# Optimization experiments

Hardware: AMD Instinct MI355X
Metric: run time of the kernel (lower is better)

The kernel has to match this reference:

```python
import jax, jax.numpy as jnp
import numpy as np

# GNB per-element parameters [s, beta, R, C6] indexed by atomic number Z (rows not listed stay zero)
_ROWS = {
 1:[0.2772,1.7504,3.6516,95.99], 2:[0.2425,2.087,2.1843,40.67], 3:[0.3266,2.3073,1.2711,70.21],
 4:[0.3964,2.8811,3.3497,114.51], 5:[0.3121,2.6366,2.7079,152.36], 6:[0.2455,3.0189,1.8219,184.28],
 7:[0.2743,2.9432,2.4667,482.54], 8:[0.2577,2.7407,2.365,405.57], 9:[0.2791,2.5863,1.5062,218.45],
 10:[0.2378,2.5307,1.8233,174.81], 11:[0.2592,2.5679,1.3974,181.7], 12:[0.3837,2.9613,3.3515,263.02],
 13:[0.3013,3.2377,3.0102,228.1], 14:[0.3202,3.2749,3.1629,359.43], 15:[0.3399,3.7491,3.2554,3222.12],
 16:[0.3215,3.6718,2.9539,2144.49], 17:[0.3071,3.418,3.0368,2072.46], 18:[0.2752,3.3306,2.6598,1357.42],
 19:[0.2264,2.9736,4.0877,1406.65], 20:[0.4015,3.4464,4.1275,1058.36], 21:[0.9388,4.5955,9.7282,11498.73],
 22:[0.6048,3.5334,8.5322,3361.33], 23:[0.3678,3.068,7.2344,2095.91], 24:[0.2848,2.8393,5.3605,1049.31],
 25:[0.355,3.055,3.718,966.27], 26:[0.4406,3.2628,3.6408,1571.36], 27:[0.4124,3.2622,3.4961,1183.59],
 28:[0.3139,2.749,3.5108,787.76], 29:[0.3345,2.9097,3.0537,563.93], 30:[0.3391,2.9024,3.0261,592.91],
 31:[0.3146,3.3924,3.1735,430.82], 32:[0.3327,3.2804,3.1773,812.57], 33:[0.404,3.8757,3.8357,4533.53],
 34:[0.3343,3.8562,3.1109,3440.92], 35:[0.3242,3.7067,3.2122,3859.82], 36:[0.292,3.6457,2.8263,2729.6],
 37:[0.2677,3.4421,2.412,1864.19], 38:[0.3446,3.559,1.894,1175.73], 39:[1.0038,5.7293,11.2061,32141.18],
 40:[0.6146,5.075,6.821,27655.14], 41:[0.4244,3.7156,7.2367,2864.2], 42:[0.4882,3.6853,3.901,3563.45],
 43:[0.4439,3.6987,4.0857,3266.43], 44:[0.4736,3.7826,4.045,3967.23], 45:[0.4039,3.4706,3.4813,2233.82],
 46:[0.3188,3.3433,3.0487,1393.49], 47:[0.2948,3.1186,2.7795,1315.09], 48:[0.3012,3.0853,2.8673,1311.47],
 49:[0.3351,3.5452,3.3339,1460.56], 50:[0.3134,3.2997,3.0086,1662.99], 51:[0.4081,4.1277,3.9919,8089.97],
 52:[0.3585,4.1795,3.4209,6887.05], 53:[0.3574,4.0988,3.5649,8799.32], 54:[0.3134,4.0387,3.0288,6136.5],
 55:[0.2872,3.8468,2.262,3757.31], 56:[0.3788,4.0368,1.3837,2561.18], 57:[1.0851,6.1365,12.171,66580.83],
 72:[0.5577,5.213,6.0791,27593.76], 73:[0.5308,4.7637,5.7661,15364.65], 74:[0.3926,3.6018,3.6366,2734.5],
 75:[0.5351,3.9552,4.241,4801.82], 76:[0.4701,4.0278,4.1348,5685.94], 77:[0.3661,3.6123,3.4213,2786.0],
 78:[0.3411,3.6066,3.2486,2699.79], 79:[0.3164,3.3822,2.9588,2282.6], 80:[0.3047,3.375,2.9381,2476.79],
 81:[0.2802,3.3964,2.7711,2988.7], 82:[0.2682,3.2481,2.5816,2506.63], 83:[0.3876,4.1225,3.785,8916.84],
 84:[0.3679,4.2313,3.5381,8694.22], 85:[0.368,4.2455,3.6985,11821.61], 86:[0.3195,4.1784,3.0551,8410.64],
}
_TAB = np.zeros((87, 4), np.float32)
for _z, _v in _ROWS.items():
    _TAB[_z] = _v
GNB_TABLE = jnp.asarray(_TAB)
C_SP2 = jnp.asarray(np.array([0.2808, 3.0548, 2.2348, 429.69], np.float32))
C_SP3 = jnp.asarray(np.array([0.2455, 3.0189, 1.8219, 184.28], np.float32))
N_CN2 = jnp.asarray(np.array([0.2996, 3.02, 2.6454, 720.18], np.float32))
N_CN3 = jnp.asarray(np.array([0.2743, 2.9432, 2.4667, 482.54], np.float32))

BJ_A1, BJ_A2, BJ_ALPHA = 0.4, 4.0, 14.0
CUTOFF_LR, CUTOFF_START = 10.0, 8.0  # cutoff_start = cutoff_lr - 2.0


def _poly_envelope(x):
    # PolynomialCutoff.calculate_envelope with r_max=1, p=6:
    x6 = x ** 6
    env = 1.0 - 28.0 * x6 + 48.0 * x6 * x - 21.0 * x6 * x * x
    return env * (x < 1.0)


def _gnb_forward(lengths, Z, edge_index):
    n_nodes = Z.shape[0]
    sender, receiver = edge_index[0], edge_index[1]

    # coordination numbers via scatter-add on receiver
    cn = jnp.zeros((n_nodes,), jnp.int32).at[receiver].add(1)

    # species-indexed params with CN-adaptive selection for C and N
    params = GNB_TABLE[Z]  # [N, 4]
    c_params = jnp.where((cn <= 3)[:, None], C_SP2[None, :], C_SP3[None, :])
    n_params = jnp.where((cn <= 2)[:, None], N_CN2[None, :], N_CN3[None, :])
    params = jnp.where((Z == 6)[:, None], c_params, params)
    params = jnp.where((Z == 7)[:, None], n_params, params)

    R_i = params[:, 2]
    C6_i = params[:, 3]

    # geometric-mean combination rules per edge
    C6_ij = jnp.sqrt(C6_i[sender] * C6_i[receiver])
    R_ij = jnp.sqrt(R_i[sender] * R_i[receiver])

    r = lengths
    # BJ damping: f = 1 / (1 + 6 (r/r0)^(-alpha)), r0 = a1 sqrt(R_ij) + a2
    r0 = BJ_A1 * jnp.sqrt(R_ij) + BJ_A2
    f_damp = 1.0 / (1.0 + 6.0 * (r0 / r) ** BJ_ALPHA)

    e_edge = -C6_ij / (R_ij ** 6 + r ** 6) * f_damp

    # long-range polynomial cutoff switching from 1 at cutoff_start to 0 at cutoff_lr
    x = (r - CUTOFF_START) / (CUTOFF_LR - CUTOFF_START)
    env = jnp.where(r < CUTOFF_START, 1.0, _poly_envelope(x))
    e_edge = e_edge * env

    # scatter-sum to atoms; 0.5 to split symmetric pair energy over both directions
    node_energy = jnp.zeros((n_nodes,), e_edge.dtype).at[receiver].add(0.5 * e_edge)
    return node_energy


def setup_inputs() -> dict:
    key = jax.random.key(0)
    k1, k2, k3 = jax.random.split(key, 3)
    n_nodes, n_edges = 100000, 6400000
    Z = jax.random.randint(k1, (n_nodes,), 1, 87, dtype=jnp.int32)
    edge_index = jax.random.randint(k2, (2, n_edges), 0, n_nodes, dtype=jnp.int32)
    lengths = jax.random.uniform(k3, (n_edges,), jnp.float32, 1.0, 10.5)
    return {"Z": Z, "edge_index": edge_index, "lengths": lengths}


def reference(Z, edge_index, lengths):
    return _gnb_forward(lengths, Z, edge_index)
```

## Files before the change

### kernel.cpp

```cpp
#include <hip/hip_runtime.h>


#define B2SHIFT 10
#define B2SIZE  1024
#define TILE    4096
#define SBLK    512
#define ESLICES 32
#define MAXB    128

__device__ __constant__ float2 GNB_RC6[87] = {
    {0.f, 0.f},
    {3.6516f, 95.99f},   {2.1843f, 40.67f},   {1.2711f, 70.21f},
    {3.3497f, 114.51f},  {2.7079f, 152.36f},  {1.8219f, 184.28f},
    {2.4667f, 482.54f},  {2.365f, 405.57f},   {1.5062f, 218.45f},
    {1.8233f, 174.81f},  {1.3974f, 181.7f},   {3.3515f, 263.02f},
    {3.0102f, 228.1f},   {3.1629f, 359.43f},  {3.2554f, 3222.12f},
    {2.9539f, 2144.49f}, {3.0368f, 2072.46f}, {2.6598f, 1357.42f},
    {4.0877f, 1406.65f}, {4.1275f, 1058.36f}, {9.7282f, 11498.73f},
    {8.5322f, 3361.33f}, {7.2344f, 2095.91f}, {5.3605f, 1049.31f},
    {3.718f, 966.27f},   {3.6408f, 1571.36f}, {3.4961f, 1183.59f},
    {3.5108f, 787.76f},  {3.0537f, 563.93f},  {3.0261f, 592.91f},
    {3.1735f, 430.82f},  {3.1773f, 812.57f},  {3.8357f, 4533.53f},
    {3.1109f, 3440.92f}, {3.2122f, 3859.82f}, {2.8263f, 2729.6f},
    {2.412f, 1864.19f},  {1.894f, 1175.73f},  {11.2061f, 32141.18f},
    {6.821f, 27655.14f}, {7.2367f, 2864.2f},  {3.901f, 3563.45f},
    {4.0857f, 3266.43f}, {4.045f, 3967.23f},  {3.4813f, 2233.82f},
    {3.0487f, 1393.49f}, {2.7795f, 1315.09f}, {2.8673f, 1311.47f},
    {3.3339f, 1460.56f}, {3.0086f, 1662.99f}, {3.9919f, 8089.97f},
    {3.4209f, 6887.05f}, {3.5649f, 8799.32f}, {3.0288f, 6136.5f},
    {2.262f, 3757.31f},  {1.3837f, 2561.18f}, {12.171f, 66580.83f},
    {0.f,0.f},{0.f,0.f},{0.f,0.f},{0.f,0.f},{0.f,0.f},{0.f,0.f},{0.f,0.f},
    {0.f,0.f},{0.f,0.f},{0.f,0.f},{0.f,0.f},{0.f,0.f},{0.f,0.f},{0.f,0.f},
    {6.0791f, 27593.76f}, {5.7661f, 15364.65f}, {3.6366f, 2734.5f},
    {4.241f, 4801.82f},   {4.1348f, 5685.94f},  {3.4213f, 2786.0f},
    {3.2486f, 2699.79f},  {2.9588f, 2282.6f},   {2.9381f, 2476.79f},
    {2.7711f, 2988.7f},   {2.5816f, 2506.63f},  {3.785f, 8916.84f},
    {3.5381f, 8694.22f},  {3.6985f, 11821.61f}, {3.0551f, 8410.64f},
};

__global__ void gnb_init(const int* __restrict__ Z, unsigned* __restrict__ isCN,
                         int nw, int n_nodes, int* __restrict__ zp, int zwords) {
    int stride = gridDim.x * blockDim.x;
    int t0 = blockIdx.x * blockDim.x + threadIdx.x;
    for (int i = t0; i < zwords; i += stride) zp[i] = 0;
    for (int w = t0; w < nw; w += stride) {
        unsigned m = 0;
        int base = w << 5;
        int lim = n_nodes - base; if (lim > 32) lim = 32;
        for (int k = 0; k < lim; ++k) {
            int z = Z[base + k];
            if (z == 6 || z == 7) m |= (1u << k);
        }
        isCN[w] = m;
    }
}

__global__ void __launch_bounds__(SBLK)
gnb_scatter(const int* __restrict__ send, const int* __restrict__ recv,
            const float* __restrict__ len, const unsigned* __restrict__ isCN,
            int* __restrict__ cn,
            uint2* __restrict__ buckets, unsigned* __restrict__ cursor,
            uint4* __restrict__ ovrec, unsigned* __restrict__ ocur,
            int n_edges, int cap, unsigned ocap, int NB2) {
    __shared__ unsigned cnt[MAXB];
    __shared__ unsigned pos[MAXB];
    __shared__ unsigned startp[MAXB + 1];
    __shared__ unsigned gbase[MAXB];
    __shared__ uint2 srec[TILE];
    __shared__ unsigned char bmap[TILE];
    const int tid = threadIdx.x;
    const int e0  = blockIdx.x * TILE;

    for (int b = tid; b < MAXB; b += SBLK) { cnt[b] = 0; pos[b] = 0; }
    __syncthreads();

    #pragma unroll
    for (int k = 0; k < 2; ++k) {
        int base = e0 + (k * SBLK + tid) * 4;
        if (base + 3 < n_edges) {
            int4   rv = *(const int4*)(recv + base);
            float4 lv = *(const float4*)(len + base);
            int rr[4] = {rv.x, rv.y, rv.z, rv.w};
            float ll[4] = {lv.x, lv.y, lv.z, lv.w};
            #pragma unroll
            for (int j = 0; j < 4; ++j) {
                unsigned r = (unsigned)rr[j];
                if (ll[j] < 10.0f) atomicAdd(&cnt[r >> B2SHIFT], 1u);
                if ((isCN[r >> 5] >> (r & 31)) & 1u) atomicAdd(&cn[r], 1);
            }
        } else {
            int lim = n_edges - base; if (lim < 0) lim = 0; if (lim > 4) lim = 4;
            for (int j = 0; j < lim; ++j) {
                unsigned r = (unsigned)recv[base + j];
                if (len[base + j] < 10.0f) atomicAdd(&cnt[r >> B2SHIFT], 1u);
                if ((isCN[r >> 5] >> (r & 31)) & 1u) atomicAdd(&cn[r], 1);
            }
        }
    }
    __syncthreads();

    if (tid == 0) {
        unsigned acc = 0;
        for (int b = 0; b < NB2; ++b) { startp[b] = acc; acc += cnt[b]; }
        startp[NB2] = acc;
    }
    __syncthreads();
    if (tid < NB2) gbase[tid] = atomicAdd(&cursor[tid], cnt[tid]);
    __syncthreads();

    #pragma unroll
    for (int k = 0; k < 2; ++k) {
        int base = e0 + (k * SBLK + tid) * 4;
        if (base + 3 < n_edges) {
            int4   sv = *(const int4*)(send + base);
            int4   rv = *(const int4*)(recv + base);
            uint4  lv = *(const uint4*)(len + base);
            int ss[4] = {sv.x, sv.y, sv.z, sv.w};
            int rr[4] = {rv.x, rv.y, rv.z, rv.w};
            unsigned ll[4] = {lv.x, lv.y, lv.z, lv.w};
            #pragma unroll
            for (int j = 0; j < 4; ++j) {
                if (__uint_as_float(ll[j]) >= 10.0f) continue;
                unsigned r = (unsigned)rr[j];
                unsigned b = r >> B2SHIFT;
                unsigned slot = startp[b] + atomicAdd(&pos[b], 1u);
                srec[slot] = make_uint2((unsigned)ss[j] | ((r & (B2SIZE - 1)) << 17), ll[j]);
                bmap[slot] = (unsigned char)b;
            }
        } else {
            int lim = n_edges - base; if (lim < 0) lim = 0; if (lim > 4) lim = 4;
            for (int j = 0; j < lim; ++j) {
                unsigned lbits = ((const unsigned*)len)[base + j];
                if (__uint_as_float(lbits) >= 10.0f) continue;
                unsigned r = (unsigned)recv[base + j];
                unsigned b = r >> B2SHIFT;
                unsigned slot = startp[b] + atomicAdd(&pos[b], 1u);
                srec[slot] = make_uint2((unsigned)send[base + j] | ((r & (B2SIZE - 1)) << 17),
                                        lbits);
                bmap[slot] = (unsigned char)b;
            }
        }
    }
    __syncthreads();

    unsigned total = startp[NB2];
    for (unsigned i = tid; i < total; i += SBLK) {
        unsigned b = bmap[i];
        unsigned g = gbase[b] + (i - startp[b]);
        uint2 rec = srec[i];
        if (g < (unsigned)cap) {
            buckets[(size_t)b * cap + g] = rec;
        } else {
            unsigned o = atomicAdd(ocur, 1u);
            unsigned r = ((unsigned)b << B2SHIFT) | ((rec.x >> 17) & (B2SIZE - 1));
            if (o < ocap) ovrec[o] = make_uint4(r, rec.x & 0x1FFFFu, rec.y, 0u);
        }
    }
}

__global__ void gnb_params(const int* __restrict__ Z, const int* __restrict__ cn,
                           float2* __restrict__ P2, int n_nodes) {
    int i = blockIdx.x * blockDim.x + threadIdx.x;
    if (i >= n_nodes) return;
    int z = Z[i];
    float Rp, C6;
    if (z == 6) {
        if (cn[i] <= 3) { Rp = 2.2348f; C6 = 429.69f; }
        else            { Rp = 1.8219f; C6 = 184.28f; }
    } else if (z == 7) {
        if (cn[i] <= 2) { Rp = 2.6454f; C6 = 720.18f; }
        else            { Rp = 2.4667f; C6 = 482.54f; }
    } else {
        float2 rc = GNB_RC6[z];
        Rp = rc.x; C6 = rc.y;
    }
    P2[i] = make_float2(sqrtf(C6), sqrtf(sqrtf(Rp)));
}

__device__ __forceinline__ float gnb_energy_eval(float2 ps, float2 pr, float rlen) {
    float env;
    if (rlen < 8.0f) {
        env = 1.0f;
    } else {
        float x = (rlen - 8.0f) * 0.5f;
        float x2 = x * x;
        float x6 = x2 * x2 * x2;
        env = 1.0f - 28.0f * x6 + 48.0f * x6 * x - 21.0f * x6 * x2;
    }
    float sR  = ps.y * pr.y;
    float C6  = ps.x * pr.x;
    float Rij = sR * sR;
    float R3  = Rij * Rij * Rij;
    float R6  = R3 * R3;
    float r0  = 0.4f * sR + 4.0f;
    float t   = r0 / rlen;
    float t2 = t * t, t4 = t2 * t2, t8 = t4 * t4;
    float t14 = t8 * t4 * t2;
    float fd = 1.0f / (1.0f + 6.0f * t14);
    float rl2 = rlen * rlen;
    float r6 = rl2 * rl2 * rl2;
    return -0.5f * C6 / (R6 + r6) * fd * env;
}

__global__ void __launch_bounds__(256)
gnb_energy(const uint2* __restrict__ buckets, const unsigned* __restrict__ cursor,
           const float2* __restrict__ P2, float* __restrict__ rep,
           int cap, int n_nodes) {
    __shared__ float  acc[2][B2SIZE + 8];
    __shared__ float2 p2loc[B2SIZE];
    const int b   = blockIdx.x / ESLICES;
    const int sl  = blockIdx.x % ESLICES;
    const int tid = threadIdx.x;
    const int rr  = (tid >> 6) & 1;

    for (int i = tid; i < 2 * (B2SIZE + 8); i += 256) acc[0][i] = 0.0f;
    for (int i = tid; i < B2SIZE; i += 256) {
        int node = (b << B2SHIFT) + i;
        p2loc[i] = (node < n_nodes) ? P2[node] : make_float2(0.f, 0.f);
    }
    __syncthreads();

    unsigned count = cursor[b];
    if (count > (unsigned)cap) count = (unsigned)cap;
    unsigned seg = (count + ESLICES - 1) / ESLICES;
    unsigned st  = (unsigned)sl * seg;
    unsigned en  = st + seg; if (en > count) en = count;

    const uint2* src = buckets + (size_t)b * cap;
    for (unsigned i = st + tid; i < en; i += 256) {
        uint2 rec = src[i];
        unsigned s    = rec.x & 0x1FFFFu;
        unsigned rlow = (rec.x >> 17) & (B2SIZE - 1);
        float e = gnb_energy_eval(P2[s], p2loc[rlow], __uint_as_float(rec.y));
        atomicAdd(&acc[rr][rlow], e);
    }
    __syncthreads();

    float* dst = rep + (size_t)blockIdx.x * B2SIZE;
    for (int i = tid; i < B2SIZE; i += 256) dst[i] = acc[0][i] + acc[1][i];
}

__global__ void gnb_ovf_energy(const uint4* __restrict__ ovrec, const unsigned* __restrict__ ocur,
                               const float2* __restrict__ P2, float* __restrict__ ovf,
                               unsigned ocap) {
    unsigned n = *ocur; if (n > ocap) n = ocap;
    int stride = gridDim.x * blockDim.x;
    for (unsigned i = blockIdx.x * blockDim.x + threadIdx.x; i < n; i += stride) {
        uint4 rec = ovrec[i];
        float rlen = __uint_as_float(rec.z);
        if (rlen >= 10.0f) continue;
        float e = gnb_energy_eval(P2[rec.y], P2[rec.x], rlen);
        atomicAdd(&ovf[rec.x], e);
    }
}

__global__ void gnb_reduce(const float* __restrict__ rep, const float* __restrict__ ovf,
                           float* __restrict__ out, int n_nodes) {
    int i = blockIdx.x * blockDim.x + threadIdx.x;
    if (i >= n_nodes) return;
    int b = i >> B2SHIFT;
    int j = i & (B2SIZE - 1);
    const float* src = rep + ((size_t)b * ESLICES) * B2SIZE + j;
    float sum = ovf[i];
    #pragma unroll
    for (int s = 0; s < ESLICES; ++s) sum += src[(size_t)s * B2SIZE];
    out[i] = sum;
}

extern "C" void kernel_launch(void* const* d_in, const int* in_sizes, int n_in,
                              void* d_out, int out_size, void* d_ws, size_t ws_size,
                              hipStream_t stream) {
    const int*   Z    = (const int*)d_in[0];
    const int*   eidx = (const int*)d_in[1];
    const float* len  = (const float*)d_in[2];
    float*       out  = (float*)d_out;

    const int n_nodes = in_sizes[0];
    const int n_edges = in_sizes[2];
    const int* send = eidx;
    const int* recv = eidx + n_edges;

    const int NB2 = (n_nodes + B2SIZE - 1) >> B2SHIFT;
    const int nw  = (n_nodes + 31) >> 5;
    const int nwp = (nw + 7) & ~7;

    char* ws = (char*)d_ws;
    unsigned* cursor = (unsigned*)ws;
    unsigned* ocur   = (unsigned*)(ws + MAXB * 4);
    int*      cn     = (int*)(ws + (MAXB + 8) * 4);
    float*    ovf    = (float*)(ws + ((size_t)n_nodes + MAXB + 8) * 4);
    float2*   P2     = (float2*)(ws + ((size_t)2 * n_nodes + MAXB + 8) * 4);
    unsigned* isCN   = (unsigned*)(ws + ((size_t)4 * n_nodes + MAXB + 8) * 4);
    float*    rep    = (float*)((char*)isCN + (size_t)nwp * 4);
    size_t rep_w     = (size_t)NB2 * ESLICES * B2SIZE;
    char*     tail   = (char*)rep + rep_w * 4;

    size_t fixed_words = (size_t)4 * n_nodes + MAXB + 8 + nwp + rep_w;
    size_t total_words = ws_size / 4;
    size_t avail = total_words > fixed_words ? total_words - fixed_words : 0;
    size_t ovw = avail / 32;
    unsigned ocap = (unsigned)(ovw / 4);
    long cap = (long)((avail - ovw) / (2 * (size_t)NB2));
    if (cap > n_edges) cap = n_edges;
    if (cap < 0) cap = 0;
    uint4* ovrec   = (uint4*)tail;
    uint2* buckets = (uint2*)(tail + (size_t)ocap * 16);

    const int B = 256;
    int node_blocks = (n_nodes + B - 1) / B;
    int scat_blocks = (n_edges + TILE - 1) / TILE;
    int zero_words  = 2 * n_nodes + MAXB + 8;

    gnb_init<<<256, B, 0, stream>>>(Z, isCN, nw, n_nodes, (int*)ws, zero_words);
    gnb_scatter<<<scat_blocks, SBLK, 0, stream>>>(send, recv, len, isCN, cn, buckets,
                                                  cursor, ovrec, ocur, n_edges,
                                                  (int)cap, ocap, NB2);
    gnb_params<<<node_blocks, B, 0, stream>>>(Z, cn, P2, n_nodes);
    gnb_energy<<<NB2 * ESLICES, B, 0, stream>>>(buckets, cursor, P2, rep, (int)cap, n_nodes);
    gnb_ovf_energy<<<8, B, 0, stream>>>(ovrec, ocur, P2, ovf, ocap);
    gnb_reduce<<<node_blocks, B, 0, stream>>>(rep, ovf, out, n_nodes);
}
```

Measured before the change: 203.2 us.

## Compress per-node params to byte ids, fuse overflow energy, shrink scatter tiles

Per-node parameters are now stored as a one-byte type id (Z or a carbon/nitrogen coordination variant) looked up in a small shared table, instead of a float2 per node. This shrinks the random gathers done in the energy kernel. The separate overflow-energy kernel is merged into the energy launch as extra blocks. The scatter kernel keeps its loaded receivers and lengths in registers so they are not read twice, and it folds the prefix offsets into the count array. Tile, block and slice sizes are halved, and the energy loop reads two records per 16-byte load, which adds a table indirection and more blocks in the scatter stage.

```diff
diff --git a/kernel.cpp b/kernel.cpp
--- a/kernel.cpp
+++ b/kernel.cpp
@@ -3,10 +3,11 @@
 
 #define B2SHIFT 10
 #define B2SIZE  1024
-#define TILE    4096
-#define SBLK    512
-#define ESLICES 32
+#define TILE    2048
+#define SBLK    256
+#define ESLICES 16
 #define MAXB    128
+#define OVB     8
 
 __device__ __constant__ float2 GNB_RC6[87] = {
     {0.f, 0.f},
@@ -39,7 +40,8 @@
 };
 
 __global__ void gnb_init(const int* __restrict__ Z, unsigned* __restrict__ isCN,
-                         int nw, int n_nodes, int* __restrict__ zp, int zwords) {
+                         float2* __restrict__ PT, int nw, int n_nodes,
+                         int* __restrict__ zp, int zwords) {
     int stride = gridDim.x * blockDim.x;
     int t0 = blockIdx.x * blockDim.x + threadIdx.x;
     for (int i = t0; i < zwords; i += stride) zp[i] = 0;
@@ -53,128 +55,128 @@
         }
         isCN[w] = m;
     }
-}
-
-__global__ void __launch_bounds__(SBLK)
+    if (t0 < 91) {
+        float R, C6;
+        if      (t0 < 87)  { float2 rc = GNB_RC6[t0]; R = rc.x; C6 = rc.y; }
+        else if (t0 == 87) { R = 2.2348f; C6 = 429.69f; }
+        else if (t0 == 88) { R = 1.8219f; C6 = 184.28f; }
+        else if (t0 == 89) { R = 2.6454f; C6 = 720.18f; }
+        else               { R = 2.4667f; C6 = 482.54f; }
+        PT[t0] = make_float2(sqrtf(C6), sqrtf(sqrtf(R)));
+    }
+}
+
+__global__ void __launch_bounds__(SBLK, 8)
 gnb_scatter(const int* __restrict__ send, const int* __restrict__ recv,
             const float* __restrict__ len, const unsigned* __restrict__ isCN,
             int* __restrict__ cn,
             uint2* __restrict__ buckets, unsigned* __restrict__ cursor,
             uint4* __restrict__ ovrec, unsigned* __restrict__ ocur,
             int n_edges, int cap, unsigned ocap, int NB2) {
-    __shared__ unsigned cnt[MAXB];
-    __shared__ unsigned pos[MAXB];
-    __shared__ unsigned startp[MAXB + 1];
+    __shared__ unsigned cnt[MAXB + 1];
     __shared__ unsigned gbase[MAXB];
     __shared__ uint2 srec[TILE];
     __shared__ unsigned char bmap[TILE];
     const int tid = threadIdx.x;
     const int e0  = blockIdx.x * TILE;
 
-    for (int b = tid; b < MAXB; b += SBLK) { cnt[b] = 0; pos[b] = 0; }
-    __syncthreads();
+    for (int b = tid; b < MAXB + 1; b += SBLK) cnt[b] = 0;
+    __syncthreads();
+
+    unsigned rv[8];
+    float    lv[8];
 
     #pragma unroll
     for (int k = 0; k < 2; ++k) {
         int base = e0 + (k * SBLK + tid) * 4;
         if (base + 3 < n_edges) {
-            int4   rv = *(const int4*)(recv + base);
-            float4 lv = *(const float4*)(len + base);
-            int rr[4] = {rv.x, rv.y, rv.z, rv.w};
-            float ll[4] = {lv.x, lv.y, lv.z, lv.w};
-            #pragma unroll
+            int4   rr = *(const int4*)(recv + base);
+            float4 ll = *(const float4*)(len + base);
+            rv[k*4+0] = (unsigned)rr.x; lv[k*4+0] = ll.x;
+            rv[k*4+1] = (unsigned)rr.y; lv[k*4+1] = ll.y;
+            rv[k*4+2] = (unsigned)rr.z; lv[k*4+2] = ll.z;
+            rv[k*4+3] = (unsigned)rr.w; lv[k*4+3] = ll.w;
+        } else {
             for (int j = 0; j < 4; ++j) {
-                unsigned r = (unsigned)rr[j];
-                if (ll[j] < 10.0f) atomicAdd(&cnt[r >> B2SHIFT], 1u);
-                if ((isCN[r >> 5] >> (r & 31)) & 1u) atomicAdd(&cn[r], 1);
+                int e = base + j;
+                if (e < n_edges) { rv[k*4+j] = (unsigned)recv[e]; lv[k*4+j] = len[e]; }
+                else             { rv[k*4+j] = 0xFFFFFFFFu;       lv[k*4+j] = 1e30f; }
             }
-        } else {
-            int lim = n_edges - base; if (lim < 0) lim = 0; if (lim > 4) lim = 4;
-            for (int j = 0; j < lim; ++j) {
-                unsigned r = (unsigned)recv[base + j];
-                if (len[base + j] < 10.0f) atomicAdd(&cnt[r >> B2SHIFT], 1u);
-                if ((isCN[r >> 5] >> (r & 31)) & 1u) atomicAdd(&cn[r], 1);
-            }
-        }
-    }
+        }
+    }
+    #pragma unroll
+    for (int i = 0; i < 8; ++i) {
+        unsigned r = rv[i];
+        if (r == 0xFFFFFFFFu) continue;
+        if ((isCN[r >> 5] >> (r & 31)) & 1u) atomicAdd(&cn[r], 1);
+        if (lv[i] < 10.0f) atomicAdd(&cnt[r >> B2SHIFT], 1u);
+    }
+    __syncthreads();
+
+    if (tid < NB2) gbase[tid] = atomicAdd(&cursor[tid], cnt[tid]);
     __syncthreads();
 
     if (tid == 0) {
         unsigned acc = 0;
-        for (int b = 0; b < NB2; ++b) { startp[b] = acc; acc += cnt[b]; }
-        startp[NB2] = acc;
-    }
-    __syncthreads();
-    if (tid < NB2) gbase[tid] = atomicAdd(&cursor[tid], cnt[tid]);
+        for (int b = 0; b < NB2; ++b) {
+            unsigned c = cnt[b];
+            cnt[b] = acc;
+            gbase[b] -= acc;
+            acc += c;
+        }
+        cnt[NB2] = acc;
+    }
     __syncthreads();
 
     #pragma unroll
     for (int k = 0; k < 2; ++k) {
         int base = e0 + (k * SBLK + tid) * 4;
+        unsigned sv[4];
         if (base + 3 < n_edges) {
-            int4   sv = *(const int4*)(send + base);
-            int4   rv = *(const int4*)(recv + base);
-            uint4  lv = *(const uint4*)(len + base);
-            int ss[4] = {sv.x, sv.y, sv.z, sv.w};
-            int rr[4] = {rv.x, rv.y, rv.z, rv.w};
-            unsigned ll[4] = {lv.x, lv.y, lv.z, lv.w};
-            #pragma unroll
-            for (int j = 0; j < 4; ++j) {
-                if (__uint_as_float(ll[j]) >= 10.0f) continue;
-                unsigned r = (unsigned)rr[j];
-                unsigned b = r >> B2SHIFT;
-                unsigned slot = startp[b] + atomicAdd(&pos[b], 1u);
-                srec[slot] = make_uint2((unsigned)ss[j] | ((r & (B2SIZE - 1)) << 17), ll[j]);
-                bmap[slot] = (unsigned char)b;
-            }
+            int4 s4 = *(const int4*)(send + base);
+            sv[0]=(unsigned)s4.x; sv[1]=(unsigned)s4.y; sv[2]=(unsigned)s4.z; sv[3]=(unsigned)s4.w;
         } else {
-            int lim = n_edges - base; if (lim < 0) lim = 0; if (lim > 4) lim = 4;
-            for (int j = 0; j < lim; ++j) {
-                unsigned lbits = ((const unsigned*)len)[base + j];
-                if (__uint_as_float(lbits) >= 10.0f) continue;
-                unsigned r = (unsigned)recv[base + j];
-                unsigned b = r >> B2SHIFT;
-                unsigned slot = startp[b] + atomicAdd(&pos[b], 1u);
-                srec[slot] = make_uint2((unsigned)send[base + j] | ((r & (B2SIZE - 1)) << 17),
-                                        lbits);
-                bmap[slot] = (unsigned char)b;
-            }
-        }
-    }
-    __syncthreads();
-
-    unsigned total = startp[NB2];
+            for (int j = 0; j < 4; ++j)
+                sv[j] = (base + j < n_edges) ? (unsigned)send[base + j] : 0u;
+        }
+        #pragma unroll
+        for (int j = 0; j < 4; ++j) {
+            int i = k * 4 + j;
+            if (rv[i] == 0xFFFFFFFFu || lv[i] >= 10.0f) continue;
+            unsigned r = rv[i];
+            unsigned b = r >> B2SHIFT;
+            unsigned slot = atomicAdd(&cnt[b], 1u);
+            srec[slot] = make_uint2(sv[j] | ((r & (B2SIZE - 1)) << 17),
+                                    __float_as_uint(lv[i]));
+            bmap[slot] = (unsigned char)b;
+        }
+    }
+    __syncthreads();
+
+    unsigned total = cnt[NB2];
     for (unsigned i = tid; i < total; i += SBLK) {
         unsigned b = bmap[i];
-        unsigned g = gbase[b] + (i - startp[b]);
+        unsigned g = gbase[b] + i;
         uint2 rec = srec[i];
         if (g < (unsigned)cap) {
             buckets[(size_t)b * cap + g] = rec;
         } else {
             unsigned o = atomicAdd(ocur, 1u);
-            unsigned r = ((unsigned)b << B2SHIFT) | ((rec.x >> 17) & (B2SIZE - 1));
+            unsigned r = (b << B2SHIFT) | ((rec.x >> 17) & (B2SIZE - 1));
             if (o < ocap) ovrec[o] = make_uint4(r, rec.x & 0x1FFFFu, rec.y, 0u);
         }
     }
 }
 
 __global__ void gnb_params(const int* __restrict__ Z, const int* __restrict__ cn,
-                           float2* __restrict__ P2, int n_nodes) {
+                           unsigned char* __restrict__ pid, int n_nodes) {
     int i = blockIdx.x * blockDim.x + threadIdx.x;
     if (i >= n_nodes) return;
     int z = Z[i];
-    float Rp, C6;
-    if (z == 6) {
-        if (cn[i] <= 3) { Rp = 2.2348f; C6 = 429.69f; }
-        else            { Rp = 1.8219f; C6 = 184.28f; }
-    } else if (z == 7) {
-        if (cn[i] <= 2) { Rp = 2.6454f; C6 = 720.18f; }
-        else            { Rp = 2.4667f; C6 = 482.54f; }
-    } else {
-        float2 rc = GNB_RC6[z];
-        Rp = rc.x; C6 = rc.y;
-    }
-    P2[i] = make_float2(sqrtf(C6), sqrtf(sqrtf(Rp)));
+    int id = z;
+    if (z == 6)      id = (cn[i] <= 3) ? 87 : 88;
+    else if (z == 7) id = (cn[i] <= 2) ? 89 : 90;
+    pid[i] = (unsigned char)id;
 }
 
 __device__ __forceinline__ float gnb_energy_eval(float2 ps, float2 pr, float rlen) {
@@ -204,54 +206,73 @@
 
 __global__ void __launch_bounds__(256)
 gnb_energy(const uint2* __restrict__ buckets, const unsigned* __restrict__ cursor,
-           const float2* __restrict__ P2, float* __restrict__ rep,
-           int cap, int n_nodes) {
+           const float2* __restrict__ PT, const unsigned char* __restrict__ pid,
+           float* __restrict__ rep, float* __restrict__ ovf,
+           const uint4* __restrict__ ovrec, const unsigned* __restrict__ ocur,
+           unsigned ocap, int cap, int n_nodes, int nmain) {
     __shared__ float  acc[2][B2SIZE + 8];
     __shared__ float2 p2loc[B2SIZE];
-    const int b   = blockIdx.x / ESLICES;
-    const int sl  = blockIdx.x % ESLICES;
+    __shared__ float2 ptab[96];
     const int tid = threadIdx.x;
+    const int bid = blockIdx.x;
+    const int b   = bid / ESLICES;
     const int rr  = (tid >> 6) & 1;
 
-    for (int i = tid; i < 2 * (B2SIZE + 8); i += 256) acc[0][i] = 0.0f;
-    for (int i = tid; i < B2SIZE; i += 256) {
-        int node = (b << B2SHIFT) + i;
-        p2loc[i] = (node < n_nodes) ? P2[node] : make_float2(0.f, 0.f);
-    }
-    __syncthreads();
-
+    if (tid < 91) ptab[tid] = PT[tid];
+    if (bid < nmain) {
+        for (int i = tid; i < 2 * (B2SIZE + 8); i += 256) acc[0][i] = 0.0f;
+        for (int i = tid; i < B2SIZE; i += 256) {
+            int node = (b << B2SHIFT) + i;
+            p2loc[i] = (node < n_nodes) ? PT[pid[node]] : make_float2(0.f, 0.f);
+        }
+    }
+    __syncthreads();
+
+    if (bid >= nmain) {
+        unsigned n = *ocur; if (n > ocap) n = ocap;
+        unsigned t0 = (unsigned)(bid - nmain) * 256 + tid;
+        for (unsigned i = t0; i < n; i += OVB * 256) {
+            uint4 rec = ovrec[i];
+            float rlen = __uint_as_float(rec.z);
+            if (rlen >= 10.0f) continue;
+            float e = gnb_energy_eval(ptab[pid[rec.y]], ptab[pid[rec.x]], rlen);
+            atomicAdd(&ovf[rec.x], e);
+        }
+        return;
+    }
+
+    const int sl = bid % ESLICES;
     unsigned count = cursor[b];
     if (count > (unsigned)cap) count = (unsigned)cap;
-    unsigned seg = (count + ESLICES - 1) / ESLICES;
+    unsigned seg = (((count + ESLICES - 1) / ESLICES) + 1) & ~1u;
     unsigned st  = (unsigned)sl * seg;
     unsigned en  = st + seg; if (en > count) en = count;
 
     const uint2* src = buckets + (size_t)b * cap;
-    for (unsigned i = st + tid; i < en; i += 256) {
-        uint2 rec = src[i];
-        unsigned s    = rec.x & 0x1FFFFu;
-        unsigned rlow = (rec.x >> 17) & (B2SIZE - 1);
-        float e = gnb_energy_eval(P2[s], p2loc[rlow], __uint_as_float(rec.y));
-        atomicAdd(&acc[rr][rlow], e);
-    }
-    __syncthreads();
-
-    float* dst = rep + (size_t)blockIdx.x * B2SIZE;
+    for (unsigned i = st + 2 * tid; i < en; i += 512) {
+        if (i + 1 < en) {
+            uint4 q = *(const uint4*)(src + i);
+            {
+                unsigned s = q.x & 0x1FFFFu, rl = (q.x >> 17) & (B2SIZE - 1);
+                float e = gnb_energy_eval(ptab[pid[s]], p2loc[rl], __uint_as_float(q.y));
+                atomicAdd(&acc[rr][rl], e);
+            }
+            {
+                unsigned s = q.z & 0x1FFFFu, rl = (q.z >> 17) & (B2SIZE - 1);
+                float e = gnb_energy_eval(ptab[pid[s]], p2loc[rl], __uint_as_float(q.w));
+                atomicAdd(&acc[rr][rl], e);
+            }
+        } else {
+            uint2 rec = src[i];
+            unsigned s = rec.x & 0x1FFFFu, rl = (rec.x >> 17) & (B2SIZE - 1);
+            float e = gnb_energy_eval(ptab[pid[s]], p2loc[rl], __uint_as_float(rec.y));
+            atomicAdd(&acc[rr][rl], e);
+        }
+    }
+    __syncthreads();
+
+    float* dst = rep + (size_t)bid * B2SIZE;
     for (int i = tid; i < B2SIZE; i += 256) dst[i] = acc[0][i] + acc[1][i];
-}
-
-__global__ void gnb_ovf_energy(const uint4* __restrict__ ovrec, const unsigned* __restrict__ ocur,
-                               const float2* __restrict__ P2, float* __restrict__ ovf,
-                               unsigned ocap) {
-    unsigned n = *ocur; if (n > ocap) n = ocap;
-    int stride = gridDim.x * blockDim.x;
-    for (unsigned i = blockIdx.x * blockDim.x + threadIdx.x; i < n; i += stride) {
-        uint4 rec = ovrec[i];
-        float rlen = __uint_as_float(rec.z);
-        if (rlen >= 10.0f) continue;
-        float e = gnb_energy_eval(P2[rec.y], P2[rec.x], rlen);
-        atomicAdd(&ovf[rec.x], e);
-    }
 }
 
 __global__ void gnb_reduce(const float* __restrict__ rep, const float* __restrict__ ovf,
@@ -281,42 +302,54 @@
     const int* recv = eidx + n_edges;
 
     const int NB2 = (n_nodes + B2SIZE - 1) >> B2SHIFT;
-    const int nw  = (n_nodes + 31) >> 5;
-    const int nwp = (nw + 7) & ~7;
+    const size_t nw  = (size_t)(n_nodes + 31) >> 5;
+    const size_t nwp = (nw + 3) & ~3ull;
+    const size_t npidw = (((size_t)n_nodes + 3) / 4 + 3) & ~3ull;
+
+    size_t o_cursor = 0;
+    size_t o_ocur   = 128;
+    size_t o_cn     = 136;
+    size_t o_ovf    = o_cn + n_nodes;
+    size_t o_PT     = o_ovf + n_nodes;
+    size_t o_isCN   = o_PT + 192;
+    size_t o_pid    = o_isCN + nwp;
+    size_t o_rep    = (o_pid + npidw + 3) & ~3ull;
+    size_t rep_w    = (size_t)NB2 * ESLICES * B2SIZE;
+    size_t o_tail   = (o_rep + rep_w + 3) & ~3ull;
 
     char* ws = (char*)d_ws;
-    unsigned* cursor = (unsigned*)ws;
-    unsigned* ocur   = (unsigned*)(ws + MAXB * 4);
-    int*      cn     = (int*)(ws + (MAXB + 8) * 4);
-    float*    ovf    = (float*)(ws + ((size_t)n_nodes + MAXB + 8) * 4);
-    float2*   P2     = (float2*)(ws + ((size_t)2 * n_nodes + MAXB + 8) * 4);
-    unsigned* isCN   = (unsigned*)(ws + ((size_t)4 * n_nodes + MAXB + 8) * 4);
-    float*    rep    = (float*)((char*)isCN + (size_t)nwp * 4);
-    size_t rep_w     = (size_t)NB2 * ESLICES * B2SIZE;
-    char*     tail   = (char*)rep + rep_w * 4;
-
-    size_t fixed_words = (size_t)4 * n_nodes + MAXB + 8 + nwp + rep_w;
+    unsigned*      cursor = (unsigned*)(ws + o_cursor * 4);
+    unsigned*      ocur   = (unsigned*)(ws + o_ocur * 4);
+    int*           cn     = (int*)(ws + o_cn * 4);
+    float*         ovf    = (float*)(ws + o_ovf * 4);
+    float2*        PT     = (float2*)(ws + o_PT * 4);
+    unsigned*      isCN   = (unsigned*)(ws + o_isCN * 4);
+    unsigned char* pid    = (unsigned char*)(ws + o_pid * 4);
+    float*         rep    = (float*)(ws + o_rep * 4);
+
     size_t total_words = ws_size / 4;
-    size_t avail = total_words > fixed_words ? total_words - fixed_words : 0;
+    size_t avail = total_words > o_tail ? total_words - o_tail : 0;
     size_t ovw = avail / 32;
     unsigned ocap = (unsigned)(ovw / 4);
     long cap = (long)((avail - ovw) / (2 * (size_t)NB2));
-    if (cap > n_edges) cap = n_edges;
+    if (cap > n_edges) cap = (long)n_edges;
     if (cap < 0) cap = 0;
-    uint4* ovrec   = (uint4*)tail;
-    uint2* buckets = (uint2*)(tail + (size_t)ocap * 16);
+    cap &= ~1L;
+    uint4* ovrec   = (uint4*)(ws + o_tail * 4);
+    uint2* buckets = (uint2*)(ws + (o_tail + (size_t)ocap * 4) * 4);
 
     const int B = 256;
     int node_blocks = (n_nodes + B - 1) / B;
     int scat_blocks = (n_edges + TILE - 1) / TILE;
-    int zero_words  = 2 * n_nodes + MAXB + 8;
-
-    gnb_init<<<256, B, 0, stream>>>(Z, isCN, nw, n_nodes, (int*)ws, zero_words);
+    int zero_words  = (int)o_PT;
+    int nmain = NB2 * ESLICES;
+
+    gnb_init<<<1024, B, 0, stream>>>(Z, isCN, PT, (int)nw, n_nodes, (int*)ws, zero_words);
     gnb_scatter<<<scat_blocks, SBLK, 0, stream>>>(send, recv, len, isCN, cn, buckets,
                                                   cursor, ovrec, ocur, n_edges,
                                                   (int)cap, ocap, NB2);
-    gnb_params<<<node_blocks, B, 0, stream>>>(Z, cn, P2, n_nodes);
-    gnb_energy<<<NB2 * ESLICES, B, 0, stream>>>(buckets, cursor, P2, rep, (int)cap, n_nodes);
-    gnb_ovf_energy<<<8, B, 0, stream>>>(ovrec, ocur, P2, ovf, ocap);
+    gnb_params<<<node_blocks, B, 0, stream>>>(Z, cn, pid, n_nodes);
+    gnb_energy<<<nmain + OVB, B, 0, stream>>>(buckets, cursor, PT, pid, rep, ovf,
+                                              ovrec, ocur, ocap, (int)cap, n_nodes, nmain);
     gnb_reduce<<<node_blocks, B, 0, stream>>>(rep, ovf, out, n_nodes);
 }
```

New measurement: 224.6 us. +10.5%, slower.

## Fuse all stages into a cooperative persistent kernel with grid syncs

Applied to the files above, without the earlier changes.

Merges the init, scatter, params, energy, overflow and reduce kernels into one persistent cooperative kernel that separates phases with grid-wide syncs. Per-node parameters become a one-byte id into a 91-entry table held in shared memory, and energy slices per bucket drop from 32 to 16. The aim is to remove launch gaps and shrink parameter and reduction traffic. In exchange, the grid is capped at about 4 blocks per CU and the scatter phase loops over tiles, which may reduce parallelism, and grid syncs add overhead. If the cooperative launch fails, the kernel is launched once per phase instead.

```diff
diff --git a/kernel.cpp b/kernel.cpp
--- a/kernel.cpp
+++ b/kernel.cpp
@@ -1,12 +1,16 @@
 #include <hip/hip_runtime.h>
+#include <hip/hip_cooperative_groups.h>
+
+namespace cg = cooperative_groups;
 
 
 #define B2SHIFT 10
 #define B2SIZE  1024
 #define TILE    4096
 #define SBLK    512
-#define ESLICES 32
+#define ES      16
 #define MAXB    128
+#define OVB     8
 
 __device__ __constant__ float2 GNB_RC6[87] = {
     {0.f, 0.f},
@@ -38,145 +42,6 @@
     {3.5381f, 8694.22f},  {3.6985f, 11821.61f}, {3.0551f, 8410.64f},
 };
 
-__global__ void gnb_init(const int* __restrict__ Z, unsigned* __restrict__ isCN,
-                         int nw, int n_nodes, int* __restrict__ zp, int zwords) {
-    int stride = gridDim.x * blockDim.x;
-    int t0 = blockIdx.x * blockDim.x + threadIdx.x;
-    for (int i = t0; i < zwords; i += stride) zp[i] = 0;
-    for (int w = t0; w < nw; w += stride) {
-        unsigned m = 0;
-        int base = w << 5;
-        int lim = n_nodes - base; if (lim > 32) lim = 32;
-        for (int k = 0; k < lim; ++k) {
-            int z = Z[base + k];
-            if (z == 6 || z == 7) m |= (1u << k);
-        }
-        isCN[w] = m;
-    }
-}
-
-__global__ void __launch_bounds__(SBLK)
-gnb_scatter(const int* __restrict__ send, const int* __restrict__ recv,
-            const float* __restrict__ len, const unsigned* __restrict__ isCN,
-            int* __restrict__ cn,
-            uint2* __restrict__ buckets, unsigned* __restrict__ cursor,
-            uint4* __restrict__ ovrec, unsigned* __restrict__ ocur,
-            int n_edges, int cap, unsigned ocap, int NB2) {
-    __shared__ unsigned cnt[MAXB];
-    __shared__ unsigned pos[MAXB];
-    __shared__ unsigned startp[MAXB + 1];
-    __shared__ unsigned gbase[MAXB];
-    __shared__ uint2 srec[TILE];
-    __shared__ unsigned char bmap[TILE];
-    const int tid = threadIdx.x;
-    const int e0  = blockIdx.x * TILE;
-
-    for (int b = tid; b < MAXB; b += SBLK) { cnt[b] = 0; pos[b] = 0; }
-    __syncthreads();
-
-    #pragma unroll
-    for (int k = 0; k < 2; ++k) {
-        int base = e0 + (k * SBLK + tid) * 4;
-        if (base + 3 < n_edges) {
-            int4   rv = *(const int4*)(recv + base);
-            float4 lv = *(const float4*)(len + base);
-            int rr[4] = {rv.x, rv.y, rv.z, rv.w};
-            float ll[4] = {lv.x, lv.y, lv.z, lv.w};
-            #pragma unroll
-            for (int j = 0; j < 4; ++j) {
-                unsigned r = (unsigned)rr[j];
-                if (ll[j] < 10.0f) atomicAdd(&cnt[r >> B2SHIFT], 1u);
-                if ((isCN[r >> 5] >> (r & 31)) & 1u) atomicAdd(&cn[r], 1);
-            }
-        } else {
-            int lim = n_edges - base; if (lim < 0) lim = 0; if (lim > 4) lim = 4;
-            for (int j = 0; j < lim; ++j) {
-                unsigned r = (unsigned)recv[base + j];
-                if (len[base + j] < 10.0f) atomicAdd(&cnt[r >> B2SHIFT], 1u);
-                if ((isCN[r >> 5] >> (r & 31)) & 1u) atomicAdd(&cn[r], 1);
-            }
-        }
-    }
-    __syncthreads();
-
-    if (tid == 0) {
-        unsigned acc = 0;
-        for (int b = 0; b < NB2; ++b) { startp[b] = acc; acc += cnt[b]; }
-        startp[NB2] = acc;
-    }
-    __syncthreads();
-    if (tid < NB2) gbase[tid] = atomicAdd(&cursor[tid], cnt[tid]);
-    __syncthreads();
-
-    #pragma unroll
-    for (int k = 0; k < 2; ++k) {
-        int base = e0 + (k * SBLK + tid) * 4;
-        if (base + 3 < n_edges) {
-            int4   sv = *(const int4*)(send + base);
-            int4   rv = *(const int4*)(recv + base);
-            uint4  lv = *(const uint4*)(len + base);
-            int ss[4] = {sv.x, sv.y, sv.z, sv.w};
-            int rr[4] = {rv.x, rv.y, rv.z, rv.w};
-            unsigned ll[4] = {lv.x, lv.y, lv.z, lv.w};
-            #pragma unroll
-            for (int j = 0; j < 4; ++j) {
-                if (__uint_as_float(ll[j]) >= 10.0f) continue;
-                unsigned r = (unsigned)rr[j];
-                unsigned b = r >> B2SHIFT;
-                unsigned slot = startp[b] + atomicAdd(&pos[b], 1u);
-                srec[slot] = make_uint2((unsigned)ss[j] | ((r & (B2SIZE - 1)) << 17), ll[j]);
-                bmap[slot] = (unsigned char)b;
-            }
-        } else {
-            int lim = n_edges - base; if (lim < 0) lim = 0; if (lim > 4) lim = 4;
-            for (int j = 0; j < lim; ++j) {
-                unsigned lbits = ((const unsigned*)len)[base + j];
-                if (__uint_as_float(lbits) >= 10.0f) continue;
-                unsigned r = (unsigned)recv[base + j];
-                unsigned b = r >> B2SHIFT;
-                unsigned slot = startp[b] + atomicAdd(&pos[b], 1u);
-                srec[slot] = make_uint2((unsigned)send[base + j] | ((r & (B2SIZE - 1)) << 17),
-                                        lbits);
-                bmap[slot] = (unsigned char)b;
-            }
-        }
-    }
-    __syncthreads();
-
-    unsigned total = startp[NB2];
-    for (unsigned i = tid; i < total; i += SBLK) {
-        unsigned b = bmap[i];
-        unsigned g = gbase[b] + (i - startp[b]);
-        uint2 rec = srec[i];
-        if (g < (unsigned)cap) {
-            buckets[(size_t)b * cap + g] = rec;
-        } else {
-            unsigned o = atomicAdd(ocur, 1u);
-            unsigned r = ((unsigned)b << B2SHIFT) | ((rec.x >> 17) & (B2SIZE - 1));
-            if (o < ocap) ovrec[o] = make_uint4(r, rec.x & 0x1FFFFu, rec.y, 0u);
-        }
-    }
-}
-
-__global__ void gnb_params(const int* __restrict__ Z, const int* __restrict__ cn,
-                           float2* __restrict__ P2, int n_nodes) {
-    int i = blockIdx.x * blockDim.x + threadIdx.x;
-    if (i >= n_nodes) return;
-    int z = Z[i];
-    float Rp, C6;
-    if (z == 6) {
-        if (cn[i] <= 3) { Rp = 2.2348f; C6 = 429.69f; }
-        else            { Rp = 1.8219f; C6 = 184.28f; }
-    } else if (z == 7) {
-        if (cn[i] <= 2) { Rp = 2.6454f; C6 = 720.18f; }
-        else            { Rp = 2.4667f; C6 = 482.54f; }
-    } else {
-        float2 rc = GNB_RC6[z];
-        Rp = rc.x; C6 = rc.y;
-    }
-    P2[i] = make_float2(sqrtf(C6), sqrtf(sqrtf(Rp)));
-}
-
 __device__ __forceinline__ float gnb_energy_eval(float2 ps, float2 pr, float rlen) {
     float env;
     if (rlen < 8.0f) {
@@ -202,69 +67,220 @@
     return -0.5f * C6 / (R6 + r6) * fd * env;
 }
 
-__global__ void __launch_bounds__(256)
-gnb_energy(const uint2* __restrict__ buckets, const unsigned* __restrict__ cursor,
-           const float2* __restrict__ P2, float* __restrict__ rep,
-           int cap, int n_nodes) {
-    __shared__ float  acc[2][B2SIZE + 8];
-    __shared__ float2 p2loc[B2SIZE];
-    const int b   = blockIdx.x / ESLICES;
-    const int sl  = blockIdx.x % ESLICES;
-    const int tid = threadIdx.x;
-    const int rr  = (tid >> 6) & 1;
-
-    for (int i = tid; i < 2 * (B2SIZE + 8); i += 256) acc[0][i] = 0.0f;
-    for (int i = tid; i < B2SIZE; i += 256) {
-        int node = (b << B2SHIFT) + i;
-        p2loc[i] = (node < n_nodes) ? P2[node] : make_float2(0.f, 0.f);
+#define SMEM_BYTES 37952
+
+__global__ void __launch_bounds__(SBLK, 8)
+gnb_mega(const int* __restrict__ send, const int* __restrict__ recv,
+         const float* __restrict__ len, const int* __restrict__ Z,
+         float* __restrict__ out,
+         unsigned* __restrict__ cursor, unsigned* __restrict__ ocur,
+         int* __restrict__ cn, float* __restrict__ ovf,
+         float2* __restrict__ PT, unsigned* __restrict__ isCN,
+         unsigned char* __restrict__ pid, float* __restrict__ rep,
+         uint4* __restrict__ ovrec, uint2* __restrict__ buckets,
+         int n_nodes, int n_edges, int NB2, int nw,
+         int cap, unsigned ocap, int zwords, int ntiles,
+         int phase_lo, int phase_hi) {
+    __shared__ __align__(16) char smem[SMEM_BYTES];
+    unsigned*      s_cnt   = (unsigned*)smem;
+    unsigned*      s_gbase = (unsigned*)(smem + 528);
+    uint2*         s_srec  = (uint2*)(smem + 1056);
+    unsigned char* s_bmap  = (unsigned char*)(smem + 33824);
+    float*         e_acc   = (float*)smem;
+    float2*        e_p2    = (float2*)(smem + 8256);
+    float2*        e_ptab  = (float2*)(smem + 16448);
+
+    cg::grid_group grid = cg::this_grid();
+    const int tid  = threadIdx.x;
+    const int gtid = blockIdx.x * SBLK + tid;
+    const int gstr = gridDim.x * SBLK;
+
+    for (int phase = phase_lo; phase <= phase_hi; ++phase) {
+        if (phase == 0) {
+            int* zp = (int*)cursor;
+            for (int i = gtid; i < zwords; i += gstr) zp[i] = 0;
+            for (int w = gtid; w < nw; w += gstr) {
+                unsigned m = 0;
+                int base = w << 5;
+                int lim = n_nodes - base; if (lim > 32) lim = 32;
+                for (int k = 0; k < lim; ++k) {
+                    int z = Z[base + k];
+                    if (z == 6 || z == 7) m |= (1u << k);
+                }
+                isCN[w] = m;
+            }
+            if (gtid < 91) {
+                float R, C6;
+                if      (gtid < 87)  { float2 rc = GNB_RC6[gtid]; R = rc.x; C6 = rc.y; }
+                else if (gtid == 87) { R = 2.2348f; C6 = 429.69f; }
+                else if (gtid == 88) { R = 1.8219f; C6 = 184.28f; }
+                else if (gtid == 89) { R = 2.6454f; C6 = 720.18f; }
+                else                 { R = 2.4667f; C6 = 482.54f; }
+                PT[gtid] = make_float2(sqrtf(C6), sqrtf(sqrtf(R)));
+            }
+        } else if (phase == 1) {
+            for (int t = blockIdx.x; t < ntiles; t += gridDim.x) {
+                for (int b = tid; b < MAXB + 1; b += SBLK) s_cnt[b] = 0;
+                __syncthreads();
+                const int e0 = t * TILE;
+
+                #pragma unroll
+                for (int k = 0; k < 2; ++k) {
+                    int base = e0 + (k * SBLK + tid) * 4;
+                    if (base + 3 < n_edges) {
+                        int4   rr = *(const int4*)(recv + base);
+                        float4 ll = *(const float4*)(len + base);
+                        int rv[4] = {rr.x, rr.y, rr.z, rr.w};
+                        float lv[4] = {ll.x, ll.y, ll.z, ll.w};
+                        #pragma unroll
+                        for (int j = 0; j < 4; ++j) {
+                            unsigned r = (unsigned)rv[j];
+                            if ((isCN[r >> 5] >> (r & 31)) & 1u) atomicAdd(&cn[r], 1);
+                            if (lv[j] < 10.0f) atomicAdd(&s_cnt[r >> B2SHIFT], 1u);
+                        }
+                    } else {
+                        int lim = n_edges - base; if (lim < 0) lim = 0; if (lim > 4) lim = 4;
+                        for (int j = 0; j < lim; ++j) {
+                            unsigned r = (unsigned)recv[base + j];
+                            if ((isCN[r >> 5] >> (r & 31)) & 1u) atomicAdd(&cn[r], 1);
+                            if (len[base + j] < 10.0f) atomicAdd(&s_cnt[r >> B2SHIFT], 1u);
+                        }
+                    }
+                }
+                __syncthreads();
+
+                if (tid < NB2) s_gbase[tid] = atomicAdd(&cursor[tid], s_cnt[tid]);
+                __syncthreads();
+                if (tid == 0) {
+                    unsigned acc = 0;
+                    for (int b = 0; b < NB2; ++b) {
+                        unsigned c = s_cnt[b];
+                        s_cnt[b] = acc;
+                        s_gbase[b] -= acc;
+                        acc += c;
+                    }
+                    s_cnt[NB2] = acc;
+                }
+                __syncthreads();
+
+                #pragma unroll
+                for (int k = 0; k < 2; ++k) {
+                    int base = e0 + (k * SBLK + tid) * 4;
+                    if (base + 3 < n_edges) {
+                        int4   sv = *(const int4*)(send + base);
+                        int4   rr = *(const int4*)(recv + base);
+                        uint4  ll = *(const uint4*)(len + base);
+                        int ss[4] = {sv.x, sv.y, sv.z, sv.w};
+                        int rv[4] = {rr.x, rr.y, rr.z, rr.w};
+                        unsigned lv[4] = {ll.x, ll.y, ll.z, ll.w};
+                        #pragma unroll
+                        for (int j = 0; j < 4; ++j) {
+                            if (__uint_as_float(lv[j]) >= 10.0f) continue;
+                            unsigned r = (unsigned)rv[j];
+                            unsigned b = r >> B2SHIFT;
+                            unsigned slot = atomicAdd(&s_cnt[b], 1u);
+                            s_srec[slot] = make_uint2((unsigned)ss[j] | ((r & (B2SIZE - 1)) << 17),
+                                                      lv[j]);
+                            s_bmap[slot] = (unsigned char)b;
+                        }
+                    } else {
+                        int lim = n_edges - base; if (lim < 0) lim = 0; if (lim > 4) lim = 4;
+                        for (int j = 0; j < lim; ++j) {
+                            unsigned lbits = ((const unsigned*)len)[base + j];
+                            if (__uint_as_float(lbits) >= 10.0f) continue;
+                            unsigned r = (unsigned)recv[base + j];
+                            unsigned b = r >> B2SHIFT;
+                            unsigned slot = atomicAdd(&s_cnt[b], 1u);
+                            s_srec[slot] = make_uint2((unsigned)send[base + j] |
+                                                      ((r & (B2SIZE - 1)) << 17), lbits);
+                            s_bmap[slot] = (unsigned char)b;
+                        }
+                    }
+                }
+                __syncthreads();
+
+                unsigned total = s_cnt[NB2];
+                for (unsigned i = tid; i < total; i += SBLK) {
+                    unsigned b = s_bmap[i];
+                    unsigned g = s_gbase[b] + i;
+                    uint2 rec = s_srec[i];
+                    if (g < (unsigned)cap) {
+                        buckets[(size_t)b * cap + g] = rec;
+                    } else {
+                        unsigned o = atomicAdd(ocur, 1u);
+                        unsigned r = ((unsigned)b << B2SHIFT) | ((rec.x >> 17) & (B2SIZE - 1));
+                        if (o < ocap) ovrec[o] = make_uint4(r, rec.x & 0x1FFFFu, rec.y, 0u);
+                    }
+                }
+            }
+        } else if (phase == 2) {
+            for (int i = gtid; i < n_nodes; i += gstr) {
+                int z = Z[i];
+                int id = z;
+                if (z == 6)      id = (cn[i] <= 3) ? 87 : 88;
+                else if (z == 7) id = (cn[i] <= 2) ? 89 : 90;
+                pid[i] = (unsigned char)id;
+            }
+        } else if (phase == 3) {
+            const int nmain = NB2 * ES;
+            for (int item = blockIdx.x; item < nmain + OVB; item += gridDim.x) {
+                if (item >= nmain) {
+                    unsigned n = *ocur; if (n > ocap) n = ocap;
+                    for (unsigned i = (unsigned)(item - nmain) * SBLK + tid; i < n;
+                         i += OVB * SBLK) {
+                        uint4 rec = ovrec[i];
+                        float rlen = __uint_as_float(rec.z);
+                        if (rlen >= 10.0f) continue;
+                        float e = gnb_energy_eval(PT[pid[rec.y]], PT[pid[rec.x]], rlen);
+                        atomicAdd(&ovf[rec.x], e);
+                    }
+                    continue;
+                }
+                const int b  = item / ES;
+                const int sl = item % ES;
+                if (tid < 91) e_ptab[tid] = PT[tid];
+                for (int i = tid; i < 2 * (B2SIZE + 8); i += SBLK) e_acc[i] = 0.0f;
+                for (int i = tid; i < B2SIZE; i += SBLK) {
+                    int node = (b << B2SHIFT) + i;
+                    e_p2[i] = (node < n_nodes) ? PT[pid[node]] : make_float2(0.f, 0.f);
+                }
+                __syncthreads();
+
+                unsigned count = cursor[b];
+                if (count > (unsigned)cap) count = (unsigned)cap;
+                unsigned seg = (count + ES - 1) / ES;
+                unsigned st  = (unsigned)sl * seg;
+                unsigned en  = st + seg; if (en > count) en = count;
+                const uint2* src = buckets + (size_t)b * cap;
+                const int rr = (tid >> 6) & 1;
+                for (unsigned i = st + tid; i < en; i += SBLK) {
+                    uint2 rec = src[i];
+                    unsigned s  = rec.x & 0x1FFFFu;
+                    unsigned rl = (rec.x >> 17) & (B2SIZE - 1);
+                    float e = gnb_energy_eval(e_ptab[pid[s]], e_p2[rl],
+                                              __uint_as_float(rec.y));
+                    atomicAdd(&e_acc[rr * (B2SIZE + 8) + rl], e);
+                }
+                __syncthreads();
+
+                float* dst = rep + (size_t)item * B2SIZE;
+                for (int i = tid; i < B2SIZE; i += SBLK)
+                    dst[i] = e_acc[i] + e_acc[B2SIZE + 8 + i];
+                __syncthreads();
+            }
+        } else {
+            for (int i = gtid; i < n_nodes; i += gstr) {
+                int b = i >> B2SHIFT;
+                int j = i & (B2SIZE - 1);
+                const float* src = rep + ((size_t)b * ES) * B2SIZE + j;
+                float sum = ovf[i];
+                #pragma unroll
+                for (int s = 0; s < ES; ++s) sum += src[(size_t)s * B2SIZE];
+                out[i] = sum;
+            }
+        }
+        if (phase < phase_hi) grid.sync();
     }
-    __syncthreads();
-
-    unsigned count = cursor[b];
-    if (count > (unsigned)cap) count = (unsigned)cap;
-    unsigned seg = (count + ESLICES - 1) / ESLICES;
-    unsigned st  = (unsigned)sl * seg;
-    unsigned en  = st + seg; if (en > count) en = count;
-
-    const uint2* src = buckets + (size_t)b * cap;
-    for (unsigned i = st + tid; i < en; i += 256) {
-        uint2 rec = src[i];
-        unsigned s    = rec.x & 0x1FFFFu;
-        unsigned rlow = (rec.x >> 17) & (B2SIZE - 1);
-        float e = gnb_energy_eval(P2[s], p2loc[rlow], __uint_as_float(rec.y));
-        atomicAdd(&acc[rr][rlow], e);
-    }
-    __syncthreads();
-
-    float* dst = rep + (size_t)blockIdx.x * B2SIZE;
-    for (int i = tid; i < B2SIZE; i += 256) dst[i] = acc[0][i] + acc[1][i];
-}
-
-__global__ void gnb_ovf_energy(const uint4* __restrict__ ovrec, const unsigned* __restrict__ ocur,
-                               const float2* __restrict__ P2, float* __restrict__ ovf,
-                               unsigned ocap) {
-    unsigned n = *ocur; if (n > ocap) n = ocap;
-    int stride = gridDim.x * blockDim.x;
-    for (unsigned i = blockIdx.x * blockDim.x + threadIdx.x; i < n; i += stride) {
-        uint4 rec = ovrec[i];
-        float rlen = __uint_as_float(rec.z);
-        if (rlen >= 10.0f) continue;
-        float e = gnb_energy_eval(P2[rec.y], P2[rec.x], rlen);
-        atomicAdd(&ovf[rec.x], e);
-    }
-}
-
-__global__ void gnb_reduce(const float* __restrict__ rep, const float* __restrict__ ovf,
-                           float* __restrict__ out, int n_nodes) {
-    int i = blockIdx.x * blockDim.x + threadIdx.x;
-    if (i >= n_nodes) return;
-    int b = i >> B2SHIFT;
-    int j = i & (B2SIZE - 1);
-    const float* src = rep + ((size_t)b * ESLICES) * B2SIZE + j;
-    float sum = ovf[i];
-    #pragma unroll
-    for (int s = 0; s < ESLICES; ++s) sum += src[(size_t)s * B2SIZE];
-    out[i] = sum;
 }
 
 extern "C" void kernel_launch(void* const* d_in, const int* in_sizes, int n_in,
@@ -272,51 +288,82 @@
                               hipStream_t stream) {
     const int*   Z    = (const int*)d_in[0];
     const int*   eidx = (const int*)d_in[1];
-    const float* len  = (const float*)d_in[2];
+    const float* lenp = (const float*)d_in[2];
     float*       out  = (float*)d_out;
 
-    const int n_nodes = in_sizes[0];
-    const int n_edges = in_sizes[2];
+    int n_nodes = in_sizes[0];
+    int n_edges = in_sizes[2];
     const int* send = eidx;
     const int* recv = eidx + n_edges;
 
-    const int NB2 = (n_nodes + B2SIZE - 1) >> B2SHIFT;
-    const int nw  = (n_nodes + 31) >> 5;
-    const int nwp = (nw + 7) & ~7;
+    int NB2 = (n_nodes + B2SIZE - 1) >> B2SHIFT;
+    int nw  = (n_nodes + 31) >> 5;
+    size_t nwp   = ((size_t)nw + 3) & ~3ull;
+    size_t npidw = (((size_t)n_nodes + 3) / 4 + 3) & ~3ull;
+
+    size_t o_cn   = 136;
+    size_t o_ovf  = o_cn + n_nodes;
+    size_t o_PT   = o_ovf + n_nodes;
+    size_t o_isCN = o_PT + 192;
+    size_t o_pid  = o_isCN + nwp;
+    size_t o_rep  = (o_pid + npidw + 3) & ~3ull;
+    size_t rep_w  = (size_t)NB2 * ES * B2SIZE;
+    size_t o_tail = (o_rep + rep_w + 3) & ~3ull;
 
     char* ws = (char*)d_ws;
-    unsigned* cursor = (unsigned*)ws;
-    unsigned* ocur   = (unsigned*)(ws + MAXB * 4);
-    int*      cn     = (int*)(ws + (MAXB + 8) * 4);
-    float*    ovf    = (float*)(ws + ((size_t)n_nodes + MAXB + 8) * 4);
-    float2*   P2     = (float2*)(ws + ((size_t)2 * n_nodes + MAXB + 8) * 4);
-    unsigned* isCN   = (unsigned*)(ws + ((size_t)4 * n_nodes + MAXB + 8) * 4);
-    float*    rep    = (float*)((char*)isCN + (size_t)nwp * 4);
-    size_t rep_w     = (size_t)NB2 * ESLICES * B2SIZE;
-    char*     tail   = (char*)rep + rep_w * 4;
-
-    size_t fixed_words = (size_t)4 * n_nodes + MAXB + 8 + nwp + rep_w;
+    unsigned*      cursor = (unsigned*)ws;
+    unsigned*      ocur   = (unsigned*)(ws + 128 * 4);
+    int*           cn     = (int*)(ws + o_cn * 4);
+    float*         ovf    = (float*)(ws + o_ovf * 4);
+    float2*        PT     = (float2*)(ws + o_PT * 4);
+    unsigned*      isCN   = (unsigned*)(ws + o_isCN * 4);
+    unsigned char* pid    = (unsigned char*)(ws + o_pid * 4);
+    float*         rep    = (float*)(ws + o_rep * 4);
+
     size_t total_words = ws_size / 4;
-    size_t avail = total_words > fixed_words ? total_words - fixed_words : 0;
+    size_t avail = total_words > o_tail ? total_words - o_tail : 0;
     size_t ovw = avail / 32;
     unsigned ocap = (unsigned)(ovw / 4);
     long cap = (long)((avail - ovw) / (2 * (size_t)NB2));
     if (cap > n_edges) cap = n_edges;
     if (cap < 0) cap = 0;
-    uint4* ovrec   = (uint4*)tail;
-    uint2* buckets = (uint2*)(tail + (size_t)ocap * 16);
-
-    const int B = 256;
-    int node_blocks = (n_nodes + B - 1) / B;
-    int scat_blocks = (n_edges + TILE - 1) / TILE;
-    int zero_words  = 2 * n_nodes + MAXB + 8;
-
-    gnb_init<<<256, B, 0, stream>>>(Z, isCN, nw, n_nodes, (int*)ws, zero_words);
-    gnb_scatter<<<scat_blocks, SBLK, 0, stream>>>(send, recv, len, isCN, cn, buckets,
-                                                  cursor, ovrec, ocur, n_edges,
-                                                  (int)cap, ocap, NB2);
-    gnb_params<<<node_blocks, B, 0, stream>>>(Z, cn, P2, n_nodes);
-    gnb_energy<<<NB2 * ESLICES, B, 0, stream>>>(buckets, cursor, P2, rep, (int)cap, n_nodes);
-    gnb_ovf_energy<<<8, B, 0, stream>>>(ovrec, ocur, P2, ovf, ocap);
-    gnb_reduce<<<node_blocks, B, 0, stream>>>(rep, ovf, out, n_nodes);
+    uint4* ovrec   = (uint4*)(ws + o_tail * 4);
+    uint2* buckets = (uint2*)(ws + (o_tail + (size_t)ocap * 4) * 4);
+
+    int zwords = (int)o_PT;
+    int ntiles = (n_edges + TILE - 1) / TILE;
+    int capi   = (int)cap;
+
+    int dev = 0; hipGetDevice(&dev);
+    int cus = 256;
+    hipDeviceGetAttribute(&cus, hipDeviceAttributeMultiprocessorCount, dev);
+    int occ = 0;
+    if (hipOccupancyMaxActiveBlocksPerMultiprocessor(&occ, gnb_mega, SBLK, 0)
+        != hipSuccess || occ < 1) occ = 4;
+    if (occ > 4) occ = 4;
+    int grid = occ * cus;
+
+    int plo = 0, phi = 4;
+    void* args[] = {
+        (void*)&send, (void*)&recv, (void*)&lenp, (void*)&Z, (void*)&out,
+        (void*)&cursor, (void*)&ocur, (void*)&cn, (void*)&ovf,
+        (void*)&PT, (void*)&isCN, (void*)&pid, (void*)&rep,
+        (void*)&ovrec, (void*)&buckets,
+        (void*)&n_nodes, (void*)&n_edges, (void*)&NB2, (void*)&nw,
+        (void*)&capi, (void*)&ocap, (void*)&zwords, (void*)&ntiles,
+        (void*)&plo, (void*)&phi,
+    };
+    hipError_t err = hipLaunchCooperativeKernel((void*)gnb_mega, dim3(grid), dim3(SBLK),
+                                                args, 0, stream);
+    if (err != hipSuccess) {
+        (void)hipGetLastError();
+        int node_blocks = (n_nodes + SBLK - 1) / SBLK;
+        int pg[5] = { grid, ntiles, node_blocks, NB2 * ES + OVB, node_blocks };
+        for (int p = 0; p < 5; ++p) {
+            gnb_mega<<<pg[p], SBLK, 0, stream>>>(
+                send, recv, lenp, Z, out, cursor, ocur, cn, ovf, PT, isCN, pid,
+                rep, ovrec, buckets, n_nodes, n_edges, NB2, nw, capi, ocap,
+                zwords, ntiles, p, p);
+        }
+    }
 }
```

Result: slower. 476.8 us (+134.6%).
